# Optimization experiments

Measured on AMD Instinct MI355X. Metric: run time of the kernel, lower is better.

## Reference

```python
import jax, jax.numpy as jnp
import numpy as np
from jax import lax

B, T, C, F_IN = 32, 2048, 64, 8
CONV_F, ATT_D, HID, N_CLS = 32, 32, 128, 4


def layer_norm(x, scale, bias, eps=1e-6):
    mu = jnp.mean(x, axis=-1, keepdims=True)
    var = jnp.mean(jnp.square(x - mu), axis=-1, keepdims=True)
    return (x - mu) * lax.rsqrt(var + eps) * scale + bias


def setup_inputs() -> dict:
    key = jax.random.key(0)
    ks = jax.random.split(key, 12)
    s = lambda *sh: 1.0 / np.sqrt(sh[-2] if len(sh) > 1 else sh[-1])
    inp = {
        "X": jax.random.normal(ks[0], (B, T, C, F_IN), jnp.float32),
        "conv_w": jax.random.normal(ks[1], (5, 1, F_IN, CONV_F), jnp.float32) * 0.1,
        "conv_b": jnp.zeros((CONV_F,), jnp.float32),
        "ln1_s": jnp.ones((CONV_F,), jnp.float32),
        "ln1_b": jnp.zeros((CONV_F,), jnp.float32),
        "q_w": jax.random.normal(ks[2], (CONV_F, ATT_D), jnp.float32) * s(CONV_F, ATT_D),
        "q_b": jnp.zeros((ATT_D,), jnp.float32),
        "k_w": jax.random.normal(ks[3], (CONV_F, ATT_D), jnp.float32) * s(CONV_F, ATT_D),
        "k_b": jnp.zeros((ATT_D,), jnp.float32),
        "ca_w": jax.random.normal(ks[4], (C, C), jnp.float32) * s(C, C),
        "ca_b": jnp.zeros((C,), jnp.float32),
        "mix_w": jax.random.normal(ks[5], (C * CONV_F, HID), jnp.float32) * s(C * CONV_F, HID),
        "mix_b": jnp.zeros((HID,), jnp.float32),
        "ln2_s": jnp.ones((HID,), jnp.float32),
        "ln2_b": jnp.zeros((HID,), jnp.float32),
        "decay_logit": jnp.full((1, HID), 2.0, jnp.float32),
        "fc_w": jax.random.normal(ks[6], (HID, HID), jnp.float32) * s(HID, HID),
        "fc_b": jnp.zeros((HID,), jnp.float32),
        "out_w": jax.random.normal(ks[7], (HID, N_CLS), jnp.float32) * s(HID, N_CLS),
        "out_b": jnp.zeros((N_CLS,), jnp.float32),
        "train": False,
    }
    return inp


def reference(X, conv_w, conv_b, ln1_s, ln1_b, q_w, q_b, k_w, k_b, ca_w, ca_b,
              mix_w, mix_b, ln2_s, ln2_b, decay_logit, fc_w, fc_b, out_w, out_b, train):
    # eval mode (train=False): no input noise, dropout is identity
    # conv: (B,T,C,F_in) -> (B,T/2,C,32), SAME padding, stride (2,1)
    Xc = lax.conv_general_dilated(X, conv_w, window_strides=(2, 1), padding='SAME',
                                  dimension_numbers=('NHWC', 'HWIO', 'NHWC')) + conv_b
    Xc = jax.nn.relu(Xc)
    Xc = layer_norm(Xc, ln1_s, ln1_b)

    # dynamic graph attention over channel axis
    x_spat = jnp.mean(Xc, axis=1)                         # (B,C,32)
    q = x_spat @ q_w + q_b
    k = x_spat @ k_w + k_b
    adj = jax.nn.softmax(jnp.einsum('bcf,bdf->bcd', q, k) / jnp.sqrt(jnp.float32(ATT_D)), axis=-1)
    Xg = jnp.einsum('bcd,btdf->btcf', adj, Xc)            # (B,T2,C,32)

    # channel gating
    ca = jax.nn.sigmoid(jnp.mean(Xc, axis=(1, 3)) @ ca_w + ca_b)  # (B,C)
    Xr = Xg * ca[:, None, :, None] + Xc

    b, t2 = Xr.shape[0], Xr.shape[1]
    Xf = Xr.reshape(b, t2, -1)                            # (B,T2,2048)
    Xm = jax.nn.relu(Xf @ mix_w + mix_b)
    Xm = layer_norm(Xm, ln2_s, ln2_b)                     # (B,T2,128)

    # LIF spiking recurrence over time
    decay = jax.nn.sigmoid(decay_logit)                   # (1,128)

    def step(mem, xt):
        mem = mem * decay + xt
        spk = (mem - 0.5 > 0).astype(mem.dtype)
        mem = mem - spk * 0.5
        return mem, spk

    _, spk_seq = lax.scan(step, jnp.zeros((b, HID), Xm.dtype), jnp.swapaxes(Xm, 0, 1))
    spk_seq = jnp.swapaxes(spk_seq, 0, 1)                 # (B,T2,128)

    feat = jnp.mean(spk_seq, axis=1)                      # (B,128)
    feat = jax.nn.relu(feat @ fc_w + fc_b)
    logits = feat @ out_w + out_b
    return logits, jnp.mean(spk_seq)
```

## Files before the change

### kernel.cpp

```cpp
#include <hip/hip_runtime.h>
#include <math.h>

#define B_    32
#define T_    2048
#define T2_   1024
#define C_    64
#define FI_   8
#define FO_   32
#define K_    2048
#define H_    128

typedef unsigned short u16;
typedef short bf16x8 __attribute__((ext_vector_type(8)));
typedef float f32x4 __attribute__((ext_vector_type(4)));

#define OFF_WTH  ((size_t)67108864)
#define OFF_WTL  ((size_t)71303168)
#define OFF_XSP  ((size_t)75497472)
#define OFF_A    ((size_t)77594624)
#define OFF_XM   ((size_t)77725696)

__device__ __forceinline__ float bft(float x) {
  unsigned u = __float_as_uint(x);
  u = (u + 0x7fffu + ((u >> 16) & 1u)) & 0xffff0000u;
  return __uint_as_float(u);
}
__device__ __forceinline__ unsigned bfpack(float a, float b) {
  unsigned ua = __float_as_uint(a); ua = (ua + 0x7fffu + ((ua >> 16) & 1u)) >> 16;
  unsigned ub = __float_as_uint(b); ub = (ub + 0x7fffu + ((ub >> 16) & 1u)) & 0xffff0000u;
  return ua | ub;
}
__device__ __forceinline__ unsigned cvtpk(float a, float b) {
  unsigned r;
  asm("v_cvt_pk_bf16_f32 %0, %1, %2" : "=v"(r) : "v"(a), "v"(b));
  return r;
}

__device__ __forceinline__ void glds16(const u16* g, u16* l) {
  auto gp = reinterpret_cast<const __attribute__((address_space(1))) unsigned int*>(
      reinterpret_cast<uintptr_t>(g));
  auto lp = reinterpret_cast<__attribute__((address_space(3))) unsigned int*>(
      reinterpret_cast<uintptr_t>(l));
  __builtin_amdgcn_global_load_lds(gp, lp, 16, 0, 0);
}

__global__ __launch_bounds__(256, 4) void k1_conv_ln(
    const float* __restrict__ X, const float* __restrict__ Wc,
    const float* __restrict__ bc, const float* __restrict__ g1,
    const float* __restrict__ be1, float* __restrict__ xsp)
{
  __shared__ float xred[4][1056];
  const int tid = threadIdx.x;
  const int w = tid >> 6, lane = tid & 63;
  const int q = lane >> 4, cl = lane & 15;
  const int chalf = w & 1, rng = w >> 1;
  const int b = blockIdx.y, tile = blockIdx.x;
  const int cbase = chalf * 32;

  bf16x8 Wh[2][2], Wl[2][2];
#pragma unroll
  for (int s = 0; s < 2; ++s)
#pragma unroll
    for (int mt = 0; mt < 2; ++mt) {
      const int f = mt * 16 + cl;
      float x8[8];
#pragma unroll
      for (int j = 0; j < 8; ++j) {
        float wv;
        if (s == 0) {
          wv = Wc[(q * 8 + j) * 32 + f];
        } else {
          wv = 0.f;
          if (q == 0) wv = Wc[(32 + j) * 32 + f];
          if (q == 1 && j == 0) wv = bc[f];
        }
        x8[j] = wv;
      }
      unsigned hu[4], lu[4];
#pragma unroll
      for (int p = 0; p < 4; ++p) {
        const float a0 = x8[2*p], a1 = x8[2*p+1];
        hu[p] = bfpack(a0, a1);
        lu[p] = bfpack(a0 - bft(a0), a1 - bft(a1));
      }
      uint4 hv = make_uint4(hu[0], hu[1], hu[2], hu[3]);
      uint4 lv = make_uint4(lu[0], lu[1], lu[2], lu[3]);
      Wh[s][mt] = *(bf16x8*)&hv;
      Wl[s][mt] = *(bf16x8*)&lv;
    }

  float g1r[2][4], be1r[2][4];
#pragma unroll
  for (int mt = 0; mt < 2; ++mt)
#pragma unroll
    for (int r = 0; r < 4; ++r) {
      const int f = mt * 16 + 4 * q + r;
      g1r[mt][r] = g1[f];
      be1r[mt][r] = be1[f];
    }

  float sacc[2][2][4];
#pragma unroll
  for (int mt = 0; mt < 2; ++mt)
#pragma unroll
    for (int nt = 0; nt < 2; ++nt)
#pragma unroll
      for (int r = 0; r < 4; ++r) sacc[mt][nt][r] = 0.f;

  const float* Xb = X + (size_t)b * T_ * C_ * FI_;

#pragma unroll 1
  for (int it = 0; it < 16; ++it) {
    const int t2 = tile * 32 + rng * 16 + it;
    f32x4 acc[2][2];
#pragma unroll
    for (int mt = 0; mt < 2; ++mt)
#pragma unroll
      for (int nt = 0; nt < 2; ++nt) acc[mt][nt] = (f32x4){0.f,0.f,0.f,0.f};

#pragma unroll
    for (int nt = 0; nt < 2; ++nt) {
      const int c = cbase + nt * 16 + cl;
      const float* Xbc = Xb + (size_t)c * FI_;
      bf16x8 Bh[2], Bl[2];
      {
        const int row = 2 * t2 + q - 1;
        const bool ok = (row >= 0) && (row < T_);
        const int rc = ok ? row : 0;
        const float* p = Xbc + (size_t)rc * (C_ * FI_);
        const float4 xa = *(const float4*)p;
        const float4 xb2 = *(const float4*)(p + 4);
        float x8[8] = {xa.x, xa.y, xa.z, xa.w, xb2.x, xb2.y, xb2.z, xb2.w};
#pragma unroll
        for (int j = 0; j < 8; ++j) x8[j] = ok ? x8[j] : 0.f;
        unsigned hu[4], lu[4];
#pragma unroll
        for (int p2 = 0; p2 < 4; ++p2) {
          const float a0 = x8[2*p2], a1 = x8[2*p2+1];
          const unsigned ph = cvtpk(a0, a1);
          hu[p2] = ph;
          const float f0 = __uint_as_float(ph << 16);
          const float f1 = __uint_as_float(ph & 0xffff0000u);
          lu[p2] = cvtpk(a0 - f0, a1 - f1);
        }
        uint4 hv = make_uint4(hu[0], hu[1], hu[2], hu[3]);
        uint4 lv = make_uint4(lu[0], lu[1], lu[2], lu[3]);
        Bh[0] = *(bf16x8*)&hv; Bl[0] = *(bf16x8*)&lv;
      }
      {
        const int row = 2 * t2 + 3;
        const bool ok = (q == 0) && (row < T_);
        const int rc = ok ? row : 0;
        const float* p = Xbc + (size_t)rc * (C_ * FI_);
        const float4 xa = *(const float4*)p;
        const float4 xb2 = *(const float4*)(p + 4);
        float x8[8] = {xa.x, xa.y, xa.z, xa.w, xb2.x, xb2.y, xb2.z, xb2.w};
#pragma unroll
        for (int j = 0; j < 8; ++j) x8[j] = ok ? x8[j] : 0.f;
        unsigned hu[4], lu[4];
#pragma unroll
        for (int p2 = 0; p2 < 4; ++p2) {
          const float a0 = x8[2*p2], a1 = x8[2*p2+1];
          const unsigned ph = cvtpk(a0, a1);
          hu[p2] = ph;
          const float f0 = __uint_as_float(ph << 16);
          const float f1 = __uint_as_float(ph & 0xffff0000u);
          lu[p2] = cvtpk(a0 - f0, a1 - f1);
        }
        uint4 hv = make_uint4(hu[0], hu[1], hu[2], hu[3]);
        uint4 lv = make_uint4(lu[0], lu[1], lu[2], lu[3]);
        bf16x8 bh = *(bf16x8*)&hv, bl = *(bf16x8*)&lv;
        if (q == 1) bh[0] = (short)0x3F80;
        Bh[1] = bh; Bl[1] = bl;
      }
#pragma unroll
      for (int mt = 0; mt < 2; ++mt)
#pragma unroll
        for (int s = 0; s < 2; ++s) {
          acc[mt][nt] = __builtin_amdgcn_mfma_f32_16x16x32_bf16(Wh[s][mt], Bh[s], acc[mt][nt], 0, 0, 0);
          acc[mt][nt] = __builtin_amdgcn_mfma_f32_16x16x32_bf16(Wh[s][mt], Bl[s], acc[mt][nt], 0, 0, 0);
          acc[mt][nt] = __builtin_amdgcn_mfma_f32_16x16x32_bf16(Wl[s][mt], Bh[s], acc[mt][nt], 0, 0, 0);
        }
    }

#pragma unroll
    for (int nt = 0; nt < 2; ++nt) {
      float v[2][4];
      float s1 = 0.f, s2 = 0.f;
#pragma unroll
      for (int mt = 0; mt < 2; ++mt)
#pragma unroll
        for (int r = 0; r < 4; ++r) {
          const float vv = fmaxf(acc[mt][nt][r], 0.f);
          v[mt][r] = vv; s1 += vv; s2 = fmaf(vv, vv, s2);
        }
      s1 += __shfl_xor(s1, 16); s2 += __shfl_xor(s2, 16);
      s1 += __shfl_xor(s1, 32); s2 += __shfl_xor(s2, 32);
      const float mu = s1 * (1.f / 32.f);
      const float var = s2 * (1.f / 32.f) - mu * mu;
      const float rs = rsqrtf(var + 1e-6f);
#pragma unroll
      for (int mt = 0; mt < 2; ++mt)
#pragma unroll
        for (int r = 0; r < 4; ++r)
          sacc[mt][nt][r] += (v[mt][r] - mu) * rs * g1r[mt][r] + be1r[mt][r];
    }
  }

#pragma unroll
  for (int mt = 0; mt < 2; ++mt)
#pragma unroll
    for (int nt = 0; nt < 2; ++nt)
#pragma unroll
      for (int r = 0; r < 4; ++r)
        xred[w][(nt * 16 + cl) * 33 + mt * 16 + 4 * q + r] = sacc[mt][nt][r];
  __syncthreads();
  if (w < 2) {
#pragma unroll
    for (int mt = 0; mt < 2; ++mt)
#pragma unroll
      for (int nt = 0; nt < 2; ++nt)
#pragma unroll
        for (int r = 0; r < 4; ++r) {
          const int idx = (nt * 16 + cl) * 33 + mt * 16 + 4 * q + r;
          const float vv = xred[w][idx] + xred[w + 2][idx];
          xsp[((size_t)b * 32 + tile) * 2048 +
              (size_t)(w * 32 + nt * 16 + cl) * 32 + mt * 16 + 4 * q + r] = vv;
        }
  }
}

__global__ __launch_bounds__(256) void k2_graph(
    const float* __restrict__ xsp, const float* __restrict__ qw,
    const float* __restrict__ qb, const float* __restrict__ kw,
    const float* __restrict__ kb, const float* __restrict__ caw,
    const float* __restrict__ cab, float* __restrict__ Aout)
{
  __shared__ float xs[64 * 32];
  __shared__ float qs[64][32];
  __shared__ float ks[64][32];
  __shared__ float sc[64][64];
  __shared__ float cain[64];
  __shared__ float cav[64];
  const int tid = threadIdx.x;
  const int b = blockIdx.x;

  for (int idx = tid; idx < 2048; idx += 256) {
    float s = 0.f;
    for (int p = 0; p < 32; ++p) s += xsp[((size_t)b * 32 + p) * 2048 + idx];
    xs[idx] = s * (1.f / (float)T2_);
  }
  __syncthreads();

  if (tid < 64) {
    float s = 0.f;
#pragma unroll
    for (int f = 0; f < 32; ++f) s += xs[tid * 32 + f];
    cain[tid] = s * (1.f / 32.f);
  }
  {
    const int cc = tid >> 2, part = tid & 3;
    float aq[8], ak[8];
#pragma unroll
    for (int j = 0; j < 8; ++j) { aq[j] = qb[part*8+j]; ak[j] = kb[part*8+j]; }
    for (int f = 0; f < 32; ++f) {
      const float xv = xs[cc * 32 + f];
#pragma unroll
      for (int j = 0; j < 8; ++j) {
        aq[j] = fmaf(xv, qw[f * 32 + part*8+j], aq[j]);
        ak[j] = fmaf(xv, kw[f * 32 + part*8+j], ak[j]);
      }
    }
#pragma unroll
    for (int j = 0; j < 8; ++j) { qs[cc][part*8+j] = aq[j]; ks[cc][part*8+j] = ak[j]; }
  }
  __syncthreads();
  {
    const int cc = tid >> 2, part = tid & 3;
    for (int dd = part * 16; dd < part * 16 + 16; ++dd) {
      float s = 0.f;
#pragma unroll
      for (int e = 0; e < 32; ++e) s = fmaf(qs[cc][e], ks[dd][e], s);
      sc[cc][dd] = s * 0.1767766953f;
    }
  }
  __syncthreads();
  if (tid < 64) {
    const int cc = tid;
    float m = -1e30f;
    for (int d = 0; d < 64; ++d) m = fmaxf(m, sc[cc][d]);
    float sum = 0.f;
    for (int d = 0; d < 64; ++d) { float e = expf(sc[cc][d] - m); sc[cc][d] = e; sum += e; }
    const float inv = 1.f / sum;
    for (int d = 0; d < 64; ++d) sc[cc][d] *= inv;
    float a = cab[cc];
    for (int d = 0; d < 64; ++d) a = fmaf(cain[d], caw[d * 64 + cc], a);
    cav[cc] = 1.f / (1.f + expf(-a));
  }
  __syncthreads();
  for (int idx = tid; idx < 4096; idx += 256) {
    const int cc = idx >> 6, dd = idx & 63;
    Aout[(size_t)b * 4096 + idx] = cav[cc] * sc[cc][dd] + (cc == dd ? 1.f : 0.f);
  }
}

__global__ __launch_bounds__(256) void k3_weff(
    const float* __restrict__ Aout, const float* __restrict__ mixw,
    u16* __restrict__ Wth, u16* __restrict__ Wtl)
{
  __shared__ float Ap[4096];
  __shared__ float Ms[2048];
  const int tid = threadIdx.x;
  const int b = blockIdx.x >> 5, ht = blockIdx.x & 31;
  const int d = tid & 63, hl = tid >> 6;
  const int h0 = ht * 4;
  const float* Ab = Aout + (size_t)b * 4096;
#pragma unroll
  for (int l = 0; l < 16; ++l) Ap[tid + 256 * l] = Ab[tid + 256 * l];

  float acc[32];
#pragma unroll
  for (int j = 0; j < 32; ++j) acc[j] = 0.f;

  for (int c0 = 0; c0 < 64; c0 += 16) {
    __syncthreads();
    {
      const int i0 = tid * 8;
#pragma unroll
      for (int qd = 0; qd < 2; ++qd) {
        const int i = i0 + qd * 4;
        const int cc = i >> 7, f = (i >> 2) & 31;
        const float4 v = *(const float4*)&mixw[((size_t)((c0+cc)*32 + f))*128 + h0];
        float* mp = &Ms[cc * 128 + f];
        mp[0] = v.x; mp[32] = v.y; mp[64] = v.z; mp[96] = v.w;
      }
    }
    __syncthreads();
#pragma unroll 4
    for (int cc = 0; cc < 16; ++cc) {
      const float a = Ap[(c0 + cc) * 64 + d];
      const float* mrow = &Ms[cc * 128 + hl * 32];
#pragma unroll
      for (int fq = 0; fq < 8; ++fq) {
        const f32x4 m = *(const f32x4*)&mrow[fq * 4];
        acc[fq*4+0] = fmaf(a, m[0], acc[fq*4+0]);
        acc[fq*4+1] = fmaf(a, m[1], acc[fq*4+1]);
        acc[fq*4+2] = fmaf(a, m[2], acc[fq*4+2]);
        acc[fq*4+3] = fmaf(a, m[3], acc[fq*4+3]);
      }
    }
  }

  const int h = h0 + hl;
  const size_t obase = ((size_t)(b * 64 + d) * 128 + h) * 32;
#pragma unroll
  for (int g = 0; g < 4; ++g) {
    unsigned hq[4], lq[4];
#pragma unroll
    for (int jj = 0; jj < 4; ++jj) {
      const float ya = acc[8*g + 2*jj], yb = acc[8*g + 2*jj + 1];
      const float ha = bft(ya), hb = bft(yb);
      hq[jj] = (__float_as_uint(ha) >> 16) | (__float_as_uint(hb) & 0xffff0000u);
      lq[jj] = bfpack(ya - ha, yb - hb);
    }
    const int pg = (g ^ hl) * 8;
    *(uint4*)(Wth + obase + pg) = make_uint4(hq[0], hq[1], hq[2], hq[3]);
    *(uint4*)(Wtl + obase + pg) = make_uint4(lq[0], lq[1], lq[2], lq[3]);
  }
}

__global__ __launch_bounds__(256, 2) void k4_fused(
    const float* __restrict__ X, const float* __restrict__ Wc,
    const float* __restrict__ bc, const float* __restrict__ g1,
    const float* __restrict__ be1,
    const u16* __restrict__ Bgh, const u16* __restrict__ Bgl,
    const float* __restrict__ mixb, const float* __restrict__ g2,
    const float* __restrict__ be2, float* __restrict__ Xm)
{
  __shared__ __align__(16) u16 lds[8192 + 16384];
  __shared__ float part[64 * 8];
  __shared__ float murs[128];

  const int tid = threadIdx.x;
  const int w = tid >> 6, lane = tid & 63;
  const int q = lane >> 4, cl = lane & 15;
  const int x = blockIdx.x;
  const int swz = (x & 7) * 64 + (x >> 3);
  const int b = swz >> 4, mt = swz & 15;
  const int m0 = mt * 64;

  bf16x8 Wh[2][2], Wl[2][2];
#pragma unroll
  for (int s = 0; s < 2; ++s)
#pragma unroll
    for (int m2 = 0; m2 < 2; ++m2) {
      const int f = m2 * 16 + cl;
      float x8[8];
#pragma unroll
      for (int j = 0; j < 8; ++j) {
        float wv;
        if (s == 0) {
          wv = Wc[(q * 8 + j) * 32 + f];
        } else {
          wv = 0.f;
          if (q == 0) wv = Wc[(32 + j) * 32 + f];
          if (q == 1 && j == 0) wv = bc[f];
        }
        x8[j] = wv;
      }
      unsigned hu[4], lu[4];
#pragma unroll
      for (int p = 0; p < 4; ++p) {
        const float a0 = x8[2*p], a1 = x8[2*p+1];
        hu[p] = bfpack(a0, a1);
        lu[p] = bfpack(a0 - bft(a0), a1 - bft(a1));
      }
      uint4 hv = make_uint4(hu[0], hu[1], hu[2], hu[3]);
      uint4 lv = make_uint4(lu[0], lu[1], lu[2], lu[3]);
      Wh[s][m2] = *(bf16x8*)&hv;
      Wl[s][m2] = *(bf16x8*)&lv;
    }
  float g1r[2][4], be1r[2][4];
#pragma unroll
  for (int m2 = 0; m2 < 2; ++m2)
#pragma unroll
    for (int r = 0; r < 4; ++r) {
      const int f = m2 * 16 + 4 * q + r;
      g1r[m2][r] = g1[f];
      be1r[m2][r] = be1[f];
    }

  f32x4 acc[4][2];
#pragma unroll
  for (int i = 0; i < 4; ++i)
#pragma unroll
    for (int j = 0; j < 2; ++j) acc[i][j] = (f32x4){0.f, 0.f, 0.f, 0.f};

  const int lrow = lane >> 2, lg = lane & 3;
  const size_t brow0 = (size_t)b * 262144 + (size_t)(w * 16 + lrow) * 32 + lg * 8;
  const int dA = w * 512;
  const int fa = cl * 32 + ((q ^ (cl & 3)) * 8);
  const float* Xb = X + (size_t)b * T_ * (C_ * FI_);
  const int t2 = m0 + w * 16 + cl;
  const int t2loc = w * 16 + cl;

#define STAGE_B(kt, buf) do {                                                \
    const int bb_ = 8192 + (buf) * 8192;                                     \
    glds16(Bgh + brow0 + (size_t)(kt) * 4096,        &lds[bb_ + dA]);        \
    glds16(Bgh + brow0 + (size_t)(kt) * 4096 + 2048, &lds[bb_ + 2048 + dA]); \
    glds16(Bgl + brow0 + (size_t)(kt) * 4096,        &lds[bb_ + 4096 + dA]); \
    glds16(Bgl + brow0 + (size_t)(kt) * 4096 + 2048, &lds[bb_ + 6144 + dA]); \
  } while (0)

  float4 xa0, xa1, xb0, xb1;
  bool ok0, ok1;
  auto loadX = [&](int c) {
    const float* base = Xb + (size_t)c * FI_;
    const int r0 = 2 * t2 + q - 1;
    ok0 = (r0 >= 0) && (r0 < T_);
    const float* p0 = base + (size_t)(ok0 ? r0 : 0) * (C_ * FI_);
    xa0 = *(const float4*)p0; xa1 = *(const float4*)(p0 + 4);
    const int r1 = 2 * t2 + 3;
    ok1 = (q == 0) && (r1 < T_);
    const float* p1 = base + (size_t)(ok1 ? r1 : 0) * (C_ * FI_);
    xb0 = *(const float4*)p1; xb1 = *(const float4*)(p1 + 4);
  };

  auto convStep = [&](int nb) {
    bf16x8 Bh[2], Bl[2];
    {
      float x8[8] = {xa0.x, xa0.y, xa0.z, xa0.w, xa1.x, xa1.y, xa1.z, xa1.w};
#pragma unroll
      for (int j = 0; j < 8; ++j) x8[j] = ok0 ? x8[j] : 0.f;
      unsigned hu[4], lu[4];
#pragma unroll
      for (int p2 = 0; p2 < 4; ++p2) {
        const float a0 = x8[2*p2], a1 = x8[2*p2+1];
        const unsigned ph = cvtpk(a0, a1);
        hu[p2] = ph;
        const float f0 = __uint_as_float(ph << 16);
        const float f1 = __uint_as_float(ph & 0xffff0000u);
        lu[p2] = cvtpk(a0 - f0, a1 - f1);
      }
      uint4 hv = make_uint4(hu[0], hu[1], hu[2], hu[3]);
      uint4 lv = make_uint4(lu[0], lu[1], lu[2], lu[3]);
      Bh[0] = *(bf16x8*)&hv; Bl[0] = *(bf16x8*)&lv;
    }
    {
      float x8[8] = {xb0.x, xb0.y, xb0.z, xb0.w, xb1.x, xb1.y, xb1.z, xb1.w};
#pragma unroll
      for (int j = 0; j < 8; ++j) x8[j] = ok1 ? x8[j] : 0.f;
      unsigned hu[4], lu[4];
#pragma unroll
      for (int p2 = 0; p2 < 4; ++p2) {
        const float a0 = x8[2*p2], a1 = x8[2*p2+1];
        const unsigned ph = cvtpk(a0, a1);
        hu[p2] = ph;
        const float f0 = __uint_as_float(ph << 16);
        const float f1 = __uint_as_float(ph & 0xffff0000u);
        lu[p2] = cvtpk(a0 - f0, a1 - f1);
      }
      uint4 hv = make_uint4(hu[0], hu[1], hu[2], hu[3]);
      uint4 lv = make_uint4(lu[0], lu[1], lu[2], lu[3]);
      bf16x8 bh = *(bf16x8*)&hv, bl = *(bf16x8*)&lv;
      if (q == 1) bh[0] = (short)0x3F80;
      Bh[1] = bh; Bl[1] = bl;
    }
    f32x4 ca[2] = {(f32x4){0.f,0.f,0.f,0.f}, (f32x4){0.f,0.f,0.f,0.f}};
#pragma unroll
    for (int m2 = 0; m2 < 2; ++m2)
#pragma unroll
      for (int s = 0; s < 2; ++s) {
        ca[m2] = __builtin_amdgcn_mfma_f32_16x16x32_bf16(Wh[s][m2], Bh[s], ca[m2], 0, 0, 0);
        ca[m2] = __builtin_amdgcn_mfma_f32_16x16x32_bf16(Wh[s][m2], Bl[s], ca[m2], 0, 0, 0);
        ca[m2] = __builtin_amdgcn_mfma_f32_16x16x32_bf16(Wl[s][m2], Bh[s], ca[m2], 0, 0, 0);
      }
    float v[2][4];
    float s1 = 0.f, s2 = 0.f;
#pragma unroll
    for (int m2 = 0; m2 < 2; ++m2)
#pragma unroll
      for (int r = 0; r < 4; ++r) {
        const float vv = fmaxf(ca[m2][r], 0.f);
        v[m2][r] = vv; s1 += vv; s2 = fmaf(vv, vv, s2);
      }
    s1 += __shfl_xor(s1, 16); s2 += __shfl_xor(s2, 16);
    s1 += __shfl_xor(s1, 32); s2 += __shfl_xor(s2, 32);
    const float mu = s1 * (1.f / 32.f);
    const float var = s2 * (1.f / 32.f) - mu * mu;
    const float rs = rsqrtf(var + 1e-6f);
    const int AsB = nb * 4096;
#pragma unroll
    for (int m2 = 0; m2 < 2; ++m2) {
      float y[4];
#pragma unroll
      for (int r = 0; r < 4; ++r)
        y[r] = (v[m2][r] - mu) * rs * g1r[m2][r] + be1r[m2][r];
      const unsigned h0 = cvtpk(y[0], y[1]);
      const unsigned h1 = cvtpk(y[2], y[3]);
      const float f00 = __uint_as_float(h0 << 16);
      const float f01 = __uint_as_float(h0 & 0xffff0000u);
      const float f10 = __uint_as_float(h1 << 16);
      const float f11 = __uint_as_float(h1 & 0xffff0000u);
      const unsigned l0 = cvtpk(y[0] - f00, y[1] - f01);
      const unsigned l1 = cvtpk(y[2] - f10, y[3] - f11);
      const int pos = (((2 * m2 + (q >> 1)) ^ (cl & 3)) * 8) + (q & 1) * 4;
      *(uint2*)&lds[AsB + t2loc * 32 + pos] = make_uint2(h0, h1);
      *(uint2*)&lds[AsB + 2048 + t2loc * 32 + pos] = make_uint2(l0, l1);
    }
  };

  loadX(0);
  STAGE_B(0, 0);
  convStep(0);
  __syncthreads();

  int cur = 0;
  for (int kt = 0; kt < 64; ++kt) {
    if (kt < 63) { loadX(kt + 1); STAGE_B(kt + 1, cur ^ 1); }
    {
      const int ab = cur * 4096, bb = 8192 + cur * 8192;
      bf16x8 ah[4], al[4], bh[2], bl[2];
#pragma unroll
      for (int mf = 0; mf < 4; ++mf) {
        ah[mf] = *(const bf16x8*)&lds[ab + mf * 512 + fa];
        al[mf] = *(const bf16x8*)&lds[ab + 2048 + mf * 512 + fa];
      }
#pragma unroll
      for (int nf = 0; nf < 2; ++nf) {
        bh[nf] = *(const bf16x8*)&lds[bb + w * 1024 + nf * 512 + fa];
        bl[nf] = *(const bf16x8*)&lds[bb + 4096 + w * 1024 + nf * 512 + fa];
      }
#pragma unroll
      for (int mf = 0; mf < 4; ++mf)
#pragma unroll
        for (int nf = 0; nf < 2; ++nf) {
          acc[mf][nf] = __builtin_amdgcn_mfma_f32_16x16x32_bf16(ah[mf], bh[nf], acc[mf][nf], 0, 0, 0);
          acc[mf][nf] = __builtin_amdgcn_mfma_f32_16x16x32_bf16(ah[mf], bl[nf], acc[mf][nf], 0, 0, 0);
          acc[mf][nf] = __builtin_amdgcn_mfma_f32_16x16x32_bf16(al[mf], bh[nf], acc[mf][nf], 0, 0, 0);
        }
    }
    if (kt < 63) convStep(cur ^ 1);
    __syncthreads();
    cur ^= 1;
  }
#undef STAGE_B

  const int c0 = w * 32 + (lane & 15);
  const float bias0 = mixb[c0], bias1 = mixb[c0 + 16];
#pragma unroll
  for (int mf = 0; mf < 4; ++mf)
#pragma unroll
    for (int r = 0; r < 4; ++r) {
      float v0 = fmaxf(acc[mf][0][r] + bias0, 0.f);
      float v1 = fmaxf(acc[mf][1][r] + bias1, 0.f);
      acc[mf][0][r] = v0; acc[mf][1][r] = v1;
      float s1 = v0 + v1, s2 = v0 * v0 + v1 * v1;
      s1 += __shfl_xor(s1, 1);  s2 += __shfl_xor(s2, 1);
      s1 += __shfl_xor(s1, 2);  s2 += __shfl_xor(s2, 2);
      s1 += __shfl_xor(s1, 4);  s2 += __shfl_xor(s2, 4);
      s1 += __shfl_xor(s1, 8);  s2 += __shfl_xor(s2, 8);
      if ((lane & 15) == 0) {
        const int row = mf * 16 + (lane >> 4) * 4 + r;
        part[row * 8 + w * 2] = s1;
        part[row * 8 + w * 2 + 1] = s2;
      }
    }
  __syncthreads();
  if (tid < 64) {
    const float s1 = part[tid*8] + part[tid*8+2] + part[tid*8+4] + part[tid*8+6];
    const float s2 = part[tid*8+1] + part[tid*8+3] + part[tid*8+5] + part[tid*8+7];
    const float mu = s1 * (1.f / 128.f);
    const float var = s2 * (1.f / 128.f) - mu * mu;
    murs[tid * 2] = mu;
    murs[tid * 2 + 1] = rsqrtf(var + 1e-6f);
  }
  __syncthreads();
  const float g20 = g2[c0], g21 = g2[c0 + 16];
  const float b20 = be2[c0], b21 = be2[c0 + 16];
#pragma unroll
  for (int mf = 0; mf < 4; ++mf)
#pragma unroll
    for (int r = 0; r < 4; ++r) {
      const int row = mf * 16 + (lane >> 4) * 4 + r;
      const float mu = murs[row * 2], rs = murs[row * 2 + 1];
      float* op = Xm + (size_t)(b * 1024 + m0 + row) * 128;
      op[c0]      = (acc[mf][0][r] - mu) * rs * g20 + b20;
      op[c0 + 16] = (acc[mf][1][r] - mu) * rs * g21 + b21;
    }
}

__global__ __launch_bounds__(64) void k5_lif(
    const float* __restrict__ Xm, const float* __restrict__ dl,
    float* __restrict__ fs)
{
  const int id = blockIdx.x * 64 + threadIdx.x;
  const int b = id >> 7, h = id & 127;
  const float decay = 1.f / (1.f + expf(-dl[h]));
  float mem = 0.f, cnt = 0.f;
  const float* p = Xm + (size_t)b * T2_ * H_ + h;
#pragma unroll 16
  for (int t = 0; t < T2_; ++t) {
    const float xv = p[(size_t)t * H_];
    mem = fmaf(mem, decay, xv);
    const float sp = ((mem - 0.5f) > 0.f) ? 1.f : 0.f;
    cnt += sp;
    mem -= 0.5f * sp;
  }
  fs[b * H_ + h] = cnt;
}

__global__ __launch_bounds__(256) void k6_head(
    const float* __restrict__ fs, const float* __restrict__ fcw,
    const float* __restrict__ fcb, const float* __restrict__ ow,
    const float* __restrict__ ob, float* __restrict__ out)
{
  __shared__ float f[32 * 128];
  __shared__ float fr[32 * 128];
  __shared__ float red[256];
  const int tid = threadIdx.x;
  float tot = 0.f;
  for (int idx = tid; idx < 4096; idx += 256) {
    const float v = fs[idx];
    f[idx] = v * (1.f / (float)T2_);
    tot += v;
  }
  red[tid] = tot;
  __syncthreads();
  for (int s = 128; s > 0; s >>= 1) {
    if (tid < s) red[tid] += red[tid + s];
    __syncthreads();
  }
  {
    const int bb = tid >> 3, og = tid & 7;
    float a[16];
#pragma unroll
    for (int j = 0; j < 16; ++j) a[j] = fcb[og * 16 + j];
    for (int hh = 0; hh < 128; ++hh) {
      const float fv = f[bb * 128 + hh];
#pragma unroll
      for (int j = 0; j < 16; ++j)
        a[j] = fmaf(fv, fcw[hh * 128 + og * 16 + j], a[j]);
    }
#pragma unroll
    for (int j = 0; j < 16; ++j) fr[bb * 128 + og * 16 + j] = fmaxf(a[j], 0.f);
  }
  __syncthreads();
  if (tid < 128) {
    const int bb = tid >> 2, cls = tid & 3;
    float a = ob[cls];
    for (int o = 0; o < 128; ++o) a = fmaf(fr[bb * 128 + o], ow[o * 4 + cls], a);
    out[bb * 4 + cls] = a;
  }
  if (tid == 0) out[128] = red[0] * (1.f / (4096.f * 1024.f));
}

extern "C" void kernel_launch(void* const* d_in, const int* in_sizes, int n_in,
                              void* d_out, int out_size, void* d_ws, size_t ws_size,
                              hipStream_t stream) {
  const float* X     = (const float*)d_in[0];
  const float* convw = (const float*)d_in[1];
  const float* convb = (const float*)d_in[2];
  const float* ln1s  = (const float*)d_in[3];
  const float* ln1b  = (const float*)d_in[4];
  const float* qw    = (const float*)d_in[5];
  const float* qb    = (const float*)d_in[6];
  const float* kw    = (const float*)d_in[7];
  const float* kb    = (const float*)d_in[8];
  const float* caw   = (const float*)d_in[9];
  const float* cab   = (const float*)d_in[10];
  const float* mixw  = (const float*)d_in[11];
  const float* mixb  = (const float*)d_in[12];
  const float* ln2s  = (const float*)d_in[13];
  const float* ln2b  = (const float*)d_in[14];
  const float* dl    = (const float*)d_in[15];
  const float* fcw   = (const float*)d_in[16];
  const float* fcb   = (const float*)d_in[17];
  const float* outw  = (const float*)d_in[18];
  const float* outb  = (const float*)d_in[19];

  float* ws  = (float*)d_ws;
  u16* Wth   = (u16*)(ws + OFF_WTH);
  u16* Wtl   = (u16*)(ws + OFF_WTL);
  float* xsp = ws + OFF_XSP;
  float* Aou = ws + OFF_A;
  float* Xm  = ws + OFF_XM;
  float* fs  = ws + OFF_A;

  dim3 g1(32, 32);
  k1_conv_ln<<<g1, 256, 0, stream>>>(X, convw, convb, ln1s, ln1b, xsp);
  k2_graph<<<32, 256, 0, stream>>>(xsp, qw, qb, kw, kb, caw, cab, Aou);
  k3_weff<<<1024, 256, 0, stream>>>(Aou, mixw, Wth, Wtl);
  k4_fused<<<512, 256, 0, stream>>>(X, convw, convb, ln1s, ln1b,
                                    Wth, Wtl, mixb, ln2s, ln2b, Xm);
  k5_lif<<<64, 64, 0, stream>>>(Xm, dl, fs);
  k6_head<<<1, 256, 0, stream>>>(fs, fcw, fcb, outw, outb, (float*)d_out);
}
```

Before: 315.0 us.

## Drop low-part X split in conv, pad LDS A rows, deepen X prefetch

```diff
diff --git a/kernel.cpp b/kernel.cpp
--- a/kernel.cpp
+++ b/kernel.cpp
@@ -35,6 +35,28 @@
   asm("v_cvt_pk_bf16_f32 %0, %1, %2" : "=v"(r) : "v"(a), "v"(b));
   return r;
 }
+__device__ __forceinline__ bf16x8 packhi(const float4& x0, const float4& x1) {
+  uint4 hv = make_uint4(cvtpk(x0.x, x0.y), cvtpk(x0.z, x0.w),
+                        cvtpk(x1.x, x1.y), cvtpk(x1.z, x1.w));
+  return *(bf16x8*)&hv;
+}
+__device__ __forceinline__ void pack8(const float4& x0, const float4& x1,
+                                      bf16x8& h, bf16x8& l) {
+  float v[8] = {x0.x, x0.y, x0.z, x0.w, x1.x, x1.y, x1.z, x1.w};
+  unsigned hu[4], lu[4];
+#pragma unroll
+  for (int p = 0; p < 4; ++p) {
+    const float a = v[2*p], b2 = v[2*p+1];
+    const unsigned ph = cvtpk(a, b2);
+    hu[p] = ph;
+    const float fa_ = __uint_as_float(ph << 16);
+    const float fb_ = __uint_as_float(ph & 0xffff0000u);
+    lu[p] = cvtpk(a - fa_, b2 - fb_);
+  }
+  uint4 hv = make_uint4(hu[0], hu[1], hu[2], hu[3]);
+  uint4 lv = make_uint4(lu[0], lu[1], lu[2], lu[3]);
+  h = *(bf16x8*)&hv; l = *(bf16x8*)&lv;
+}
 
 __device__ __forceinline__ void glds16(const u16* g, u16* l) {
   auto gp = reinterpret_cast<const __attribute__((address_space(1))) unsigned int*>(
@@ -44,7 +66,7 @@
   __builtin_amdgcn_global_load_lds(gp, lp, 16, 0, 0);
 }
 
-__global__ __launch_bounds__(256, 4) void k1_conv_ln(
+__global__ __launch_bounds__(256, 3) void k1_conv_ln(
     const float* __restrict__ X, const float* __restrict__ Wc,
     const float* __restrict__ bc, const float* __restrict__ g1,
     const float* __restrict__ be1, float* __restrict__ xsp)
@@ -108,8 +130,9 @@
       for (int r = 0; r < 4; ++r) sacc[mt][nt][r] = 0.f;
 
   const float* Xb = X + (size_t)b * T_ * C_ * FI_;
-
-#pragma unroll 1
+  const float4 z4f = make_float4(0.f, 0.f, 0.f, 0.f);
+
+#pragma unroll 2
   for (int it = 0; it < 16; ++it) {
     const int t2 = tile * 32 + rng * 16 + it;
     f32x4 acc[2][2];
@@ -122,65 +145,35 @@
     for (int nt = 0; nt < 2; ++nt) {
       const int c = cbase + nt * 16 + cl;
       const float* Xbc = Xb + (size_t)c * FI_;
-      bf16x8 Bh[2], Bl[2];
+      bf16x8 Bh0, Bh1;
       {
         const int row = 2 * t2 + q - 1;
         const bool ok = (row >= 0) && (row < T_);
-        const int rc = ok ? row : 0;
-        const float* p = Xbc + (size_t)rc * (C_ * FI_);
-        const float4 xa = *(const float4*)p;
-        const float4 xb2 = *(const float4*)(p + 4);
-        float x8[8] = {xa.x, xa.y, xa.z, xa.w, xb2.x, xb2.y, xb2.z, xb2.w};
-#pragma unroll
-        for (int j = 0; j < 8; ++j) x8[j] = ok ? x8[j] : 0.f;
-        unsigned hu[4], lu[4];
-#pragma unroll
-        for (int p2 = 0; p2 < 4; ++p2) {
-          const float a0 = x8[2*p2], a1 = x8[2*p2+1];
-          const unsigned ph = cvtpk(a0, a1);
-          hu[p2] = ph;
-          const float f0 = __uint_as_float(ph << 16);
-          const float f1 = __uint_as_float(ph & 0xffff0000u);
-          lu[p2] = cvtpk(a0 - f0, a1 - f1);
+        float4 xa = z4f, xb2 = z4f;
+        if (ok) {
+          const float* p = Xbc + (size_t)row * (C_ * FI_);
+          xa = *(const float4*)p; xb2 = *(const float4*)(p + 4);
         }
-        uint4 hv = make_uint4(hu[0], hu[1], hu[2], hu[3]);
-        uint4 lv = make_uint4(lu[0], lu[1], lu[2], lu[3]);
-        Bh[0] = *(bf16x8*)&hv; Bl[0] = *(bf16x8*)&lv;
+        Bh0 = packhi(xa, xb2);
       }
       {
         const int row = 2 * t2 + 3;
         const bool ok = (q == 0) && (row < T_);
-        const int rc = ok ? row : 0;
-        const float* p = Xbc + (size_t)rc * (C_ * FI_);
-        const float4 xa = *(const float4*)p;
-        const float4 xb2 = *(const float4*)(p + 4);
-        float x8[8] = {xa.x, xa.y, xa.z, xa.w, xb2.x, xb2.y, xb2.z, xb2.w};
-#pragma unroll
-        for (int j = 0; j < 8; ++j) x8[j] = ok ? x8[j] : 0.f;
-        unsigned hu[4], lu[4];
-#pragma unroll
-        for (int p2 = 0; p2 < 4; ++p2) {
-          const float a0 = x8[2*p2], a1 = x8[2*p2+1];
-          const unsigned ph = cvtpk(a0, a1);
-          hu[p2] = ph;
-          const float f0 = __uint_as_float(ph << 16);
-          const float f1 = __uint_as_float(ph & 0xffff0000u);
-          lu[p2] = cvtpk(a0 - f0, a1 - f1);
+        float4 xa = z4f, xb2 = z4f;
+        if (ok) {
+          const float* p = Xbc + (size_t)row * (C_ * FI_);
+          xa = *(const float4*)p; xb2 = *(const float4*)(p + 4);
         }
-        uint4 hv = make_uint4(hu[0], hu[1], hu[2], hu[3]);
-        uint4 lv = make_uint4(lu[0], lu[1], lu[2], lu[3]);
-        bf16x8 bh = *(bf16x8*)&hv, bl = *(bf16x8*)&lv;
-        if (q == 1) bh[0] = (short)0x3F80;
-        Bh[1] = bh; Bl[1] = bl;
-      }
-#pragma unroll
-      for (int mt = 0; mt < 2; ++mt)
-#pragma unroll
-        for (int s = 0; s < 2; ++s) {
-          acc[mt][nt] = __builtin_amdgcn_mfma_f32_16x16x32_bf16(Wh[s][mt], Bh[s], acc[mt][nt], 0, 0, 0);
-          acc[mt][nt] = __builtin_amdgcn_mfma_f32_16x16x32_bf16(Wh[s][mt], Bl[s], acc[mt][nt], 0, 0, 0);
-          acc[mt][nt] = __builtin_amdgcn_mfma_f32_16x16x32_bf16(Wl[s][mt], Bh[s], acc[mt][nt], 0, 0, 0);
-        }
+        Bh1 = packhi(xa, xb2);
+        if (q == 1) Bh1[0] = (short)0x3F80;
+      }
+#pragma unroll
+      for (int mt = 0; mt < 2; ++mt) {
+        acc[mt][nt] = __builtin_amdgcn_mfma_f32_16x16x32_bf16(Wh[0][mt], Bh0, acc[mt][nt], 0, 0, 0);
+        acc[mt][nt] = __builtin_amdgcn_mfma_f32_16x16x32_bf16(Wl[0][mt], Bh0, acc[mt][nt], 0, 0, 0);
+        acc[mt][nt] = __builtin_amdgcn_mfma_f32_16x16x32_bf16(Wh[1][mt], Bh1, acc[mt][nt], 0, 0, 0);
+        acc[mt][nt] = __builtin_amdgcn_mfma_f32_16x16x32_bf16(Wl[1][mt], Bh1, acc[mt][nt], 0, 0, 0);
+      }
     }
 
 #pragma unroll
@@ -363,7 +356,7 @@
       hq[jj] = (__float_as_uint(ha) >> 16) | (__float_as_uint(hb) & 0xffff0000u);
       lq[jj] = bfpack(ya - ha, yb - hb);
     }
-    const int pg = (g ^ hl) * 8;
+    const int pg = (g ^ hl ^ (ht & 3)) * 8;
     *(uint4*)(Wth + obase + pg) = make_uint4(hq[0], hq[1], hq[2], hq[3]);
     *(uint4*)(Wtl + obase + pg) = make_uint4(lq[0], lq[1], lq[2], lq[3]);
   }
@@ -377,7 +370,7 @@
     const float* __restrict__ mixb, const float* __restrict__ g2,
     const float* __restrict__ be2, float* __restrict__ Xm)
 {
-  __shared__ __align__(16) u16 lds[8192 + 16384];
+  __shared__ __align__(16) u16 lds[26624];
   __shared__ float part[64 * 8];
   __shared__ float murs[128];
 
@@ -439,97 +432,60 @@
   const int lrow = lane >> 2, lg = lane & 3;
   const size_t brow0 = (size_t)b * 262144 + (size_t)(w * 16 + lrow) * 32 + lg * 8;
   const int dA = w * 512;
-  const int fa = cl * 32 + ((q ^ (cl & 3)) * 8);
+  const int faA = cl * 40 + ((q ^ (cl & 3)) * 8);
+  const int faB = cl * 32 + ((q ^ (cl & 3) ^ (cl >> 2)) * 8);
   const float* Xb = X + (size_t)b * T_ * (C_ * FI_);
   const int t2 = m0 + w * 16 + cl;
   const int t2loc = w * 16 + cl;
 
-#define STAGE_B(kt, buf) do {                                                \
-    const int bb_ = 8192 + (buf) * 8192;                                     \
-    glds16(Bgh + brow0 + (size_t)(kt) * 4096,        &lds[bb_ + dA]);        \
-    glds16(Bgh + brow0 + (size_t)(kt) * 4096 + 2048, &lds[bb_ + 2048 + dA]); \
-    glds16(Bgl + brow0 + (size_t)(kt) * 4096,        &lds[bb_ + 4096 + dA]); \
-    glds16(Bgl + brow0 + (size_t)(kt) * 4096 + 2048, &lds[bb_ + 6144 + dA]); \
-  } while (0)
-
-  float4 xa0, xa1, xb0, xb1;
-  bool ok0, ok1;
-  auto loadX = [&](int c) {
-    const float* base = Xb + (size_t)c * FI_;
-    const int r0 = 2 * t2 + q - 1;
-    ok0 = (r0 >= 0) && (r0 < T_);
-    const float* p0 = base + (size_t)(ok0 ? r0 : 0) * (C_ * FI_);
-    xa0 = *(const float4*)p0; xa1 = *(const float4*)(p0 + 4);
-    const int r1 = 2 * t2 + 3;
-    ok1 = (q == 0) && (r1 < T_);
-    const float* p1 = base + (size_t)(ok1 ? r1 : 0) * (C_ * FI_);
-    xb0 = *(const float4*)p1; xb1 = *(const float4*)(p1 + 4);
+  const int r0 = 2 * t2 + q - 1, r1 = 2 * t2 + 3;
+  const bool ok0 = (r0 >= 0) && (r0 < T_);
+  const bool ok1 = (q == 0) && (r1 < T_);
+  const float* rp0 = Xb + (size_t)(ok0 ? r0 : 0) * (C_ * FI_);
+  const float* rp1 = Xb + (size_t)(ok1 ? r1 : 0) * (C_ * FI_);
+  const float4 z4f = make_float4(0.f, 0.f, 0.f, 0.f);
+
+  float4 A0a, A1a, B0a, B1a;
+  float4 A0b, A1b, B0b, B1b;
+
+  auto LOADX = [&](float4& X0, float4& X1, float4& Y0, float4& Y1, int c) {
+    X0 = z4f; X1 = z4f; Y0 = z4f; Y1 = z4f;
+    if (ok0) { const float* p = rp0 + c * FI_; X0 = *(const float4*)p; X1 = *(const float4*)(p + 4); }
+    if (ok1) { const float* p = rp1 + c * FI_; Y0 = *(const float4*)p; Y1 = *(const float4*)(p + 4); }
   };
 
-  auto convStep = [&](int nb) {
-    bf16x8 Bh[2], Bl[2];
-    {
-      float x8[8] = {xa0.x, xa0.y, xa0.z, xa0.w, xa1.x, xa1.y, xa1.z, xa1.w};
-#pragma unroll
-      for (int j = 0; j < 8; ++j) x8[j] = ok0 ? x8[j] : 0.f;
-      unsigned hu[4], lu[4];
-#pragma unroll
-      for (int p2 = 0; p2 < 4; ++p2) {
-        const float a0 = x8[2*p2], a1 = x8[2*p2+1];
-        const unsigned ph = cvtpk(a0, a1);
-        hu[p2] = ph;
-        const float f0 = __uint_as_float(ph << 16);
-        const float f1 = __uint_as_float(ph & 0xffff0000u);
-        lu[p2] = cvtpk(a0 - f0, a1 - f1);
-      }
-      uint4 hv = make_uint4(hu[0], hu[1], hu[2], hu[3]);
-      uint4 lv = make_uint4(lu[0], lu[1], lu[2], lu[3]);
-      Bh[0] = *(bf16x8*)&hv; Bl[0] = *(bf16x8*)&lv;
-    }
-    {
-      float x8[8] = {xb0.x, xb0.y, xb0.z, xb0.w, xb1.x, xb1.y, xb1.z, xb1.w};
-#pragma unroll
-      for (int j = 0; j < 8; ++j) x8[j] = ok1 ? x8[j] : 0.f;
-      unsigned hu[4], lu[4];
-#pragma unroll
-      for (int p2 = 0; p2 < 4; ++p2) {
-        const float a0 = x8[2*p2], a1 = x8[2*p2+1];
-        const unsigned ph = cvtpk(a0, a1);
-        hu[p2] = ph;
-        const float f0 = __uint_as_float(ph << 16);
-        const float f1 = __uint_as_float(ph & 0xffff0000u);
-        lu[p2] = cvtpk(a0 - f0, a1 - f1);
-      }
-      uint4 hv = make_uint4(hu[0], hu[1], hu[2], hu[3]);
-      uint4 lv = make_uint4(lu[0], lu[1], lu[2], lu[3]);
-      bf16x8 bh = *(bf16x8*)&hv, bl = *(bf16x8*)&lv;
-      if (q == 1) bh[0] = (short)0x3F80;
-      Bh[1] = bh; Bl[1] = bl;
-    }
-    f32x4 ca[2] = {(f32x4){0.f,0.f,0.f,0.f}, (f32x4){0.f,0.f,0.f,0.f}};
-#pragma unroll
-    for (int m2 = 0; m2 < 2; ++m2)
-#pragma unroll
-      for (int s = 0; s < 2; ++s) {
-        ca[m2] = __builtin_amdgcn_mfma_f32_16x16x32_bf16(Wh[s][m2], Bh[s], ca[m2], 0, 0, 0);
-        ca[m2] = __builtin_amdgcn_mfma_f32_16x16x32_bf16(Wh[s][m2], Bl[s], ca[m2], 0, 0, 0);
-        ca[m2] = __builtin_amdgcn_mfma_f32_16x16x32_bf16(Wl[s][m2], Bh[s], ca[m2], 0, 0, 0);
-      }
+  auto CONV = [&](const float4& X0, const float4& X1,
+                  const float4& Y0, const float4& Y1, int nb) {
+    bf16x8 Bh0, Bl0, Bh1, Bl1;
+    pack8(X0, X1, Bh0, Bl0);
+    pack8(Y0, Y1, Bh1, Bl1);
+    if (q == 1) Bh1[0] = (short)0x3F80;
+    f32x4 ca0 = (f32x4){0.f,0.f,0.f,0.f}, ca1 = ca0;
+    ca0 = __builtin_amdgcn_mfma_f32_16x16x32_bf16(Wh[0][0], Bh0, ca0, 0, 0, 0);
+    ca1 = __builtin_amdgcn_mfma_f32_16x16x32_bf16(Wh[0][1], Bh0, ca1, 0, 0, 0);
+    ca0 = __builtin_amdgcn_mfma_f32_16x16x32_bf16(Wh[0][0], Bl0, ca0, 0, 0, 0);
+    ca1 = __builtin_amdgcn_mfma_f32_16x16x32_bf16(Wh[0][1], Bl0, ca1, 0, 0, 0);
+    ca0 = __builtin_amdgcn_mfma_f32_16x16x32_bf16(Wl[0][0], Bh0, ca0, 0, 0, 0);
+    ca1 = __builtin_amdgcn_mfma_f32_16x16x32_bf16(Wl[0][1], Bh0, ca1, 0, 0, 0);
+    ca0 = __builtin_amdgcn_mfma_f32_16x16x32_bf16(Wh[1][0], Bh1, ca0, 0, 0, 0);
+    ca1 = __builtin_amdgcn_mfma_f32_16x16x32_bf16(Wh[1][1], Bh1, ca1, 0, 0, 0);
+    ca0 = __builtin_amdgcn_mfma_f32_16x16x32_bf16(Wh[1][0], Bl1, ca0, 0, 0, 0);
+    ca1 = __builtin_amdgcn_mfma_f32_16x16x32_bf16(Wh[1][1], Bl1, ca1, 0, 0, 0);
+    ca0 = __builtin_amdgcn_mfma_f32_16x16x32_bf16(Wl[1][0], Bh1, ca0, 0, 0, 0);
+    ca1 = __builtin_amdgcn_mfma_f32_16x16x32_bf16(Wl[1][1], Bh1, ca1, 0, 0, 0);
     float v[2][4];
     float s1 = 0.f, s2 = 0.f;
 #pragma unroll
-    for (int m2 = 0; m2 < 2; ++m2)
-#pragma unroll
-      for (int r = 0; r < 4; ++r) {
-        const float vv = fmaxf(ca[m2][r], 0.f);
-        v[m2][r] = vv; s1 += vv; s2 = fmaf(vv, vv, s2);
-      }
+    for (int r = 0; r < 4; ++r) {
+      float vv = fmaxf(ca0[r], 0.f); v[0][r] = vv; s1 += vv; s2 = fmaf(vv, vv, s2);
+      vv = fmaxf(ca1[r], 0.f);       v[1][r] = vv; s1 += vv; s2 = fmaf(vv, vv, s2);
+    }
     s1 += __shfl_xor(s1, 16); s2 += __shfl_xor(s2, 16);
     s1 += __shfl_xor(s1, 32); s2 += __shfl_xor(s2, 32);
     const float mu = s1 * (1.f / 32.f);
     const float var = s2 * (1.f / 32.f) - mu * mu;
     const float rs = rsqrtf(var + 1e-6f);
-    const int AsB = nb * 4096;
+    const int ab = nb * 5120;
 #pragma unroll
     for (int m2 = 0; m2 < 2; ++m2) {
       float y[4];
@@ -544,45 +500,61 @@
       const float f11 = __uint_as_float(h1 & 0xffff0000u);
       const unsigned l0 = cvtpk(y[0] - f00, y[1] - f01);
       const unsigned l1 = cvtpk(y[2] - f10, y[3] - f11);
-      const int pos = (((2 * m2 + (q >> 1)) ^ (cl & 3)) * 8) + (q & 1) * 4;
-      *(uint2*)&lds[AsB + t2loc * 32 + pos] = make_uint2(h0, h1);
-      *(uint2*)&lds[AsB + 2048 + t2loc * 32 + pos] = make_uint2(l0, l1);
+      const int phys = (2 * m2 + (q >> 1)) ^ (cl & 3);
+      const int off = ab + t2loc * 40 + phys * 8 + (q & 1) * 4;
+      *(uint2*)&lds[off] = make_uint2(h0, h1);
+      *(uint2*)&lds[off + 2560] = make_uint2(l0, l1);
     }
   };
 
-  loadX(0);
+#define STAGE_B(kt, nb) do {                                                 \
+    const int bb_ = 10240 + (nb) * 8192;                                     \
+    glds16(Bgh + brow0 + (size_t)(kt) * 4096,        &lds[bb_ + dA]);        \
+    glds16(Bgh + brow0 + (size_t)(kt) * 4096 + 2048, &lds[bb_ + 2048 + dA]); \
+    glds16(Bgl + brow0 + (size_t)(kt) * 4096,        &lds[bb_ + 4096 + dA]); \
+    glds16(Bgl + brow0 + (size_t)(kt) * 4096 + 2048, &lds[bb_ + 6144 + dA]); \
+  } while (0)
+
+  auto GEMM = [&](int nb) {
+    const int ab = nb * 5120, bb = 10240 + nb * 8192;
+    bf16x8 ah[4], al[4], bh[2], bl[2];
+#pragma unroll
+    for (int mf = 0; mf < 4; ++mf) {
+      ah[mf] = *(const bf16x8*)&lds[ab + mf * 640 + faA];
+      al[mf] = *(const bf16x8*)&lds[ab + 2560 + mf * 640 + faA];
+    }
+#pragma unroll
+    for (int nf = 0; nf < 2; ++nf) {
+      bh[nf] = *(const bf16x8*)&lds[bb + w * 1024 + nf * 512 + faB];
+      bl[nf] = *(const bf16x8*)&lds[bb + 4096 + w * 1024 + nf * 512 + faB];
+    }
+#pragma unroll
+    for (int mf = 0; mf < 4; ++mf)
+#pragma unroll
+      for (int nf = 0; nf < 2; ++nf) {
+        acc[mf][nf] = __builtin_amdgcn_mfma_f32_16x16x32_bf16(ah[mf], bh[nf], acc[mf][nf], 0, 0, 0);
+        acc[mf][nf] = __builtin_amdgcn_mfma_f32_16x16x32_bf16(ah[mf], bl[nf], acc[mf][nf], 0, 0, 0);
+        acc[mf][nf] = __builtin_amdgcn_mfma_f32_16x16x32_bf16(al[mf], bh[nf], acc[mf][nf], 0, 0, 0);
+      }
+  };
+
+  LOADX(A0a, A1a, B0a, B1a, 0);
   STAGE_B(0, 0);
-  convStep(0);
-  __syncthreads();
-
-  int cur = 0;
-  for (int kt = 0; kt < 64; ++kt) {
-    if (kt < 63) { loadX(kt + 1); STAGE_B(kt + 1, cur ^ 1); }
-    {
-      const int ab = cur * 4096, bb = 8192 + cur * 8192;
-      bf16x8 ah[4], al[4], bh[2], bl[2];
-#pragma unroll
-      for (int mf = 0; mf < 4; ++mf) {
-        ah[mf] = *(const bf16x8*)&lds[ab + mf * 512 + fa];
-        al[mf] = *(const bf16x8*)&lds[ab + 2048 + mf * 512 + fa];
-      }
-#pragma unroll
-      for (int nf = 0; nf < 2; ++nf) {
-        bh[nf] = *(const bf16x8*)&lds[bb + w * 1024 + nf * 512 + fa];
-        bl[nf] = *(const bf16x8*)&lds[bb + 4096 + w * 1024 + nf * 512 + fa];
-      }
-#pragma unroll
-      for (int mf = 0; mf < 4; ++mf)
-#pragma unroll
-        for (int nf = 0; nf < 2; ++nf) {
-          acc[mf][nf] = __builtin_amdgcn_mfma_f32_16x16x32_bf16(ah[mf], bh[nf], acc[mf][nf], 0, 0, 0);
-          acc[mf][nf] = __builtin_amdgcn_mfma_f32_16x16x32_bf16(ah[mf], bl[nf], acc[mf][nf], 0, 0, 0);
-          acc[mf][nf] = __builtin_amdgcn_mfma_f32_16x16x32_bf16(al[mf], bh[nf], acc[mf][nf], 0, 0, 0);
-        }
-    }
-    if (kt < 63) convStep(cur ^ 1);
+  LOADX(A0b, A1b, B0b, B1b, 1);
+  CONV(A0a, A1a, B0a, B1a, 0);
+  __syncthreads();
+
+  for (int kt = 0; kt < 64; kt += 2) {
+    if (kt + 2 < 64) LOADX(A0a, A1a, B0a, B1a, kt + 2);
+    STAGE_B(kt + 1, 1);
+    GEMM(0);
+    CONV(A0b, A1b, B0b, B1b, 1);
     __syncthreads();
-    cur ^= 1;
+    if (kt + 3 < 64) LOADX(A0b, A1b, B0b, B1b, kt + 3);
+    if (kt + 2 < 64) STAGE_B(kt + 2, 0);
+    GEMM(1);
+    if (kt + 2 < 64) CONV(A0a, A1a, B0a, B1a, 0);
+    __syncthreads();
   }
 #undef STAGE_B
 
```

After: 307.4 us. 2.4% less time.
